# Kernel optimization log

Hardware: AMD Instinct MI355X
Metric: run time of the kernel (lower is better)

## Reference

```python
import jax, jax.numpy as jnp
import numpy as np
import math

# Model dims (from init_kwargs + mamba_ssm Mamba2 defaults)
D_MODEL = 1024
EXPAND = 2
HEADDIM = 64
D_STATE = 64
D_CONV = 4
NGROUPS = 1
D_INNER = EXPAND * D_MODEL            # 2048
NHEADS = D_INNER // HEADDIM           # 32
CONV_DIM = D_INNER + 2 * NGROUPS * D_STATE   # 2176
D_IN_PROJ = 2 * D_INNER + 2 * NGROUPS * D_STATE + NHEADS  # 4256
BATCH, SEQLEN = 4, 2048
RMS_EPS = 1.1920929e-07   # torch.finfo(float32).eps (nn.RMSNorm eps=None)
GNORM_EPS = 1e-5          # mamba_ssm RMSNormGated eps


def _rmsnorm(x, w, eps):
    return x * jax.lax.rsqrt(jnp.mean(x * x, axis=-1, keepdims=True) + eps) * w


def setup_inputs() -> dict:
    key = jax.random.key(0)
    ks = jax.random.split(key, 8)
    x = jax.random.normal(ks[0], (BATCH, SEQLEN, D_MODEL), jnp.float32)
    # router MLP (Linear(d_model,32) -> SiLU -> Linear(32,3))
    r_w1 = jax.random.normal(ks[1], (32, D_MODEL), jnp.float32) / math.sqrt(D_MODEL)
    r_b1 = jnp.zeros((32,), jnp.float32)
    r_w2 = jax.random.normal(ks[2], (3, 32), jnp.float32) / math.sqrt(32)
    r_b2 = jnp.zeros((3,), jnp.float32)
    # Mamba2 params
    in_proj_w = jax.random.normal(ks[3], (D_IN_PROJ, D_MODEL), jnp.float32) / math.sqrt(D_MODEL)
    conv_w = jax.random.normal(ks[4], (CONV_DIM, D_CONV), jnp.float32) * 0.2
    conv_b = jnp.zeros((CONV_DIM,), jnp.float32)
    dt_bias = jax.random.normal(ks[5], (NHEADS,), jnp.float32) * 0.1
    # OrthoSSM multi-scale override: A_log[i] = log(0.001 * 2**i)
    A_log = jnp.log(0.001 * (2.0 ** jnp.arange(NHEADS, dtype=jnp.float32)))
    D_param = jnp.ones((NHEADS,), jnp.float32)
    gnorm_w = jnp.ones((D_INNER,), jnp.float32)
    out_proj_w = jax.random.normal(ks[6], (D_MODEL, D_INNER), jnp.float32) / math.sqrt(D_INNER)
    norm_w = jnp.ones((D_MODEL,), jnp.float32)
    return {"x": x, "norm_w": norm_w, "r_w1": r_w1, "r_b1": r_b1, "r_w2": r_w2,
            "r_b2": r_b2, "in_proj_w": in_proj_w, "conv_w": conv_w, "conv_b": conv_b,
            "dt_bias": dt_bias, "A_log": A_log, "D_param": D_param,
            "gnorm_w": gnorm_w, "out_proj_w": out_proj_w}


def _forward(x, norm_w, r_w1, r_b1, r_w2, r_b2, in_proj_w, conv_w, conv_b,
             dt_bias, A_log, D_param, gnorm_w, out_proj_w):
    B, S, Dm = x.shape
    x_norm = _rmsnorm(x, norm_w, RMS_EPS)
    # --- router: mean-pool -> tiny MLP -> softmax over 3 tiers ---
    h = jax.nn.silu(x_norm.mean(axis=1) @ r_w1.T + r_b1)
    probs = jax.nn.softmax(h @ r_w2.T + r_b2, axis=-1)   # [B,3]
    p_fast = probs[:, 0][:, None, None]
    p_mamba = (probs[:, 1] + probs[:, 2])[:, None, None]
    # --- Mamba2(x_norm) ---
    zxbcdt = x_norm @ in_proj_w.T                         # [B,S,4256]
    z, xBC, dt = jnp.split(zxbcdt, [D_INNER, D_INNER + CONV_DIM], axis=-1)
    # causal depthwise conv1d (kernel 4) + SiLU
    conv = jax.lax.conv_general_dilated(
        xBC.transpose(0, 2, 1), conv_w[:, None, :], (1,), [(D_CONV - 1, 0)],
        feature_group_count=CONV_DIM)                      # [B,CONV_DIM,S]
    xBC = jax.nn.silu(conv.transpose(0, 2, 1) + conv_b)    # [B,S,CONV_DIM]
    xh, Bmat, Cmat = jnp.split(xBC, [D_INNER, D_INNER + NGROUPS * D_STATE], axis=-1)
    xh = xh.reshape(B, S, NHEADS, HEADDIM)                 # [B,S,H,P]
    dt = jax.nn.softplus(dt + dt_bias)                     # [B,S,H]
    A = -jnp.exp(A_log)                                    # [H]
    dA = jnp.exp(dt * A)                                   # [B,S,H]

    def step(hstate, inp):
        dA_t, dt_t, x_t, B_t, C_t = inp
        # hstate: [B,H,P,N]
        hstate = hstate * dA_t[..., None, None] \
                 + (dt_t[..., None] * x_t)[..., None] * B_t[:, None, None, :]
        y_t = jnp.einsum('bhpn,bn->bhp', hstate, C_t)
        return hstate, y_t

    h0 = jnp.zeros((B, NHEADS, HEADDIM, D_STATE), x.dtype)
    xs = (dA.transpose(1, 0, 2), dt.transpose(1, 0, 2), xh.transpose(1, 0, 2, 3),
          Bmat.transpose(1, 0, 2), Cmat.transpose(1, 0, 2))
    _, ys = jax.lax.scan(step, h0, xs)                     # [S,B,H,P]
    y = ys.transpose(1, 0, 2, 3) + D_param[:, None] * xh   # D skip connection
    y = y.reshape(B, S, D_INNER)
    # gated RMSNorm: norm(y * silu(z)) * weight
    yg = y * jax.nn.silu(z)
    yg = _rmsnorm(yg, gnorm_w, GNORM_EPS)
    mamba_out = yg @ out_proj_w.T                          # [B,S,D]
    out = p_fast * x_norm + p_mamba * mamba_out
    return x + out


def reference(x, norm_w, r_w1, r_b1, r_w2, r_b2, in_proj_w, conv_w, conv_b,
              dt_bias, A_log, D_param, gnorm_w, out_proj_w):
    return _forward(x, norm_w, r_w1, r_b1, r_w2, r_b2, in_proj_w, conv_w, conv_b,
                    dt_bias, A_log, D_param, gnorm_w, out_proj_w)
```

## Files before the change

### kernel.cpp

```cpp
#include <hip/hip_runtime.h>
#include <math.h>

typedef __bf16 bf16;
typedef __bf16 bf16x8 __attribute__((ext_vector_type(8)));
typedef __bf16 bf16x4 __attribute__((ext_vector_type(4)));
typedef float f32x4 __attribute__((ext_vector_type(4)));

#define DEV static __device__ __forceinline__
#define AS1 __attribute__((address_space(1)))
#define AS3 __attribute__((address_space(3)))

constexpr int kBatch = 4, kSeq = 2048, kDModel = 1024;
constexpr int kDInner = 2048, kHeads = 32;
constexpr int kConvDim = 2176, kDInProj = 4256, kNPad1 = 4352;
constexpr int kRows = kBatch * kSeq;
constexpr int kChunk = 64, kNChunk = kSeq / kChunk;
constexpr float kRmsEps = 1.1920929e-07f;
constexpr float kGnEps = 1e-5f;
constexpr int kW1Blocks = kNPad1 * kDModel / 256;
constexpr int kW2Blocks = kDModel * kDInner / 1024;

DEV float siluf(float x) { return x / (1.f + expf(-x)); }

DEV float block_reduce_sum(float v, float* red, int tid) {
#pragma unroll
  for (int m = 1; m < 64; m <<= 1) v += __shfl_xor(v, m);
  if ((tid & 63) == 0) red[tid >> 6] = v;
  __syncthreads();
  return red[0] + red[1] + red[2] + red[3];
}

__global__ __launch_bounds__(256) void k_pre(
    const float* __restrict__ x, const float* __restrict__ nw,
    bf16* __restrict__ xnb, float* __restrict__ rs,
    const float* __restrict__ w1, bf16* __restrict__ w1b,
    const float* __restrict__ w2, const float* __restrict__ gw,
    bf16* __restrict__ w2b) {
  const int blk = blockIdx.x;
  const int tid = threadIdx.x;
  if (blk < kRows) {
    const int row = blk;
    float4 v = ((const float4*)(x + (size_t)row * kDModel))[tid];
    __shared__ float red[4];
    float ss = block_reduce_sum(v.x * v.x + v.y * v.y + v.z * v.z + v.w * v.w, red, tid);
    float scale = rsqrtf(ss * (1.f / kDModel) + kRmsEps);
    if (tid == 0) rs[row] = scale;
    float4 wv = ((const float4*)nw)[tid];
    bf16x4 ov;
    ov[0] = (bf16)(v.x * scale * wv.x);
    ov[1] = (bf16)(v.y * scale * wv.y);
    ov[2] = (bf16)(v.z * scale * wv.z);
    ov[3] = (bf16)(v.w * scale * wv.w);
    *(bf16x4*)(xnb + (size_t)row * kDModel + tid * 4) = ov;
  } else if (blk < kRows + kW1Blocks) {
    const size_t idx = (size_t)(blk - kRows) * 256 + tid;
    const int row = (int)(idx >> 10);
    w1b[idx] = (bf16)(row < kDInProj ? w1[idx] : 0.f);
  } else {
    const size_t i4 = (size_t)(blk - kRows - kW1Blocks) * 256 + tid;
    const int k4 = (int)((i4 * 4) & (kDInner - 1));
    float4 v = ((const float4*)w2)[i4];
    float4 g = *(const float4*)(gw + k4);
    bf16x4 o;
    o[0] = (bf16)(v.x * g.x); o[1] = (bf16)(v.y * g.y);
    o[2] = (bf16)(v.z * g.z); o[3] = (bf16)(v.w * g.w);
    ((bf16x4*)w2b)[i4] = o;
  }
}

__global__ __launch_bounds__(128) void k_pool1(const bf16* __restrict__ xnb,
                                               float* __restrict__ part) {
  const int g = blockIdx.x, b = blockIdx.y;
  const int tid = threadIdx.x;
  const bf16* base = xnb + ((size_t)b * kSeq + (size_t)g * 32) * kDModel + tid * 8;
  float acc[8] = {0, 0, 0, 0, 0, 0, 0, 0};
  for (int r = 0; r < 32; ++r) {
    bf16x8 v = *(const bf16x8*)(base + (size_t)r * kDModel);
#pragma unroll
    for (int j = 0; j < 8; ++j) acc[j] += (float)v[j];
  }
  float* o = part + ((size_t)b * 64 + g) * kDModel + tid * 8;
#pragma unroll
  for (int j = 0; j < 8; ++j) o[j] = acc[j];
}

__global__ __launch_bounds__(256) void k_pool2(const float* __restrict__ part,
                                               float* __restrict__ mean) {
  const int idx = blockIdx.x * 256 + threadIdx.x;
  const int b = idx >> 10, d = idx & 1023;
  float s = 0.f;
  for (int g = 0; g < 64; ++g) s += part[((size_t)b * 64 + g) * kDModel + d];
  mean[idx] = s * (1.f / kSeq);
}

__global__ __launch_bounds__(128) void k_router(const float* __restrict__ mean,
                                                const float* __restrict__ w1,
                                                const float* __restrict__ b1,
                                                const float* __restrict__ w2,
                                                const float* __restrict__ b2,
                                                float* __restrict__ pfm) {
  __shared__ float hbuf[4][32];
  __shared__ float logit[4][3];
  const int t = threadIdx.x;
  {
    int b = t >> 5, j = t & 31;
    float s = b1[j];
    for (int d = 0; d < kDModel; ++d) s += mean[b * kDModel + d] * w1[j * kDModel + d];
    hbuf[b][j] = siluf(s);
  }
  __syncthreads();
  if (t < 12) {
    int b = t / 3, k = t % 3;
    float s = b2[k];
    for (int j = 0; j < 32; ++j) s += hbuf[b][j] * w2[k * 32 + j];
    logit[b][k] = s;
  }
  __syncthreads();
  if (t < 4) {
    float m = fmaxf(logit[t][0], fmaxf(logit[t][1], logit[t][2]));
    float e0 = expf(logit[t][0] - m), e1 = expf(logit[t][1] - m), e2 = expf(logit[t][2] - m);
    float inv = 1.f / (e0 + e1 + e2);
    pfm[t] = e0 * inv;
    pfm[4 + t] = (e1 + e2) * inv;
  }
}

template <int WM, int WN, int NF, bool FUSE>
DEV void gemm_body(bf16* lds, float* rs2s,
                   const bf16* __restrict__ A, const bf16* __restrict__ B,
                   bf16* __restrict__ Cb, const float* __restrict__ xres,
                   const float* __restrict__ rs, const float* __restrict__ nw,
                   const float* __restrict__ pfm, float* __restrict__ outf,
                   int K, int Nreal, int ldc, int ntn) {
  constexpr int THREADS = WM * WN * 64;
  constexpr int BM = WM * 64;
  constexpr int BN = WN * NF * 16;
  constexpr int NA = (BM * 4) / THREADS;
  constexpr int NB = (BN * 4) / THREADS;
  constexpr int VMN = NA + NB;
  constexpr int ASZ = (BM / 2) * 64;
  constexpr int BSZ = (BN / 2) * 64;
  const int tid = threadIdx.x;
  const int lane = tid & 63, wid = tid >> 6;
  const int wr = wid / WN, wc = wid % WN;
  const int lr = lane & 15, kb = lane >> 4;
  const int cpx = (int)gridDim.x >> 3;
  const int bid = ((int)blockIdx.x & 7) * cpx + ((int)blockIdx.x >> 3);
  const long n0 = (long)(bid % ntn) * BN;
  const long m0 = (long)(bid / ntn) * BM;

  f32x4 acc[4][NF];
#pragma unroll
  for (int i = 0; i < 4; ++i)
#pragma unroll
    for (int j = 0; j < NF; ++j) acc[i][j] = (f32x4){0.f, 0.f, 0.f, 0.f};
  float ssq[4] = {0.f, 0.f, 0.f, 0.f};

  const int nkt = K >> 5;

#define STAGE(pp, kt)                                                          \
  {                                                                            \
    const long koff = (long)(kt)*32;                                           \
    _Pragma("unroll") for (int j = 0; j < NA; ++j) {                           \
      int idx = j * THREADS + tid;                                             \
      int line = idx >> 3, sp = (idx & 7) ^ (line & 7);                        \
      int row = line * 2 + (sp >> 2), ch = sp & 3;                             \
      __builtin_amdgcn_global_load_lds(                                        \
          (const AS1 void*)(A + (m0 + row) * K + koff + ch * 8),               \
          (AS3 void*)((char*)(lds + (pp)*ASZ) + idx * 16), 16, 0, 0);          \
    }                                                                          \
    _Pragma("unroll") for (int j = 0; j < NB; ++j) {                           \
      int idx = j * THREADS + tid;                                             \
      int line = idx >> 3, sp = (idx & 7) ^ (line & 7);                        \
      int row = line * 2 + (sp >> 2), ch = sp & 3;                             \
      __builtin_amdgcn_global_load_lds(                                        \
          (const AS1 void*)(B + (n0 + row) * K + koff + ch * 8),               \
          (AS3 void*)((char*)(lds + 3 * ASZ + (pp)*BSZ) + idx * 16), 16, 0, 0);\
    }                                                                          \
  }
#define LOFF(r) (((r) >> 1) * 128 + (((((r)&1) << 2) | kb) ^ (((r) >> 1) & 7)) * 16)
#define RDA(pp, r) (*(const bf16x8*)((const char*)(lds + (pp)*ASZ) + LOFF(r)))
#define RDB(pp, r) (*(const bf16x8*)((const char*)(lds + 3 * ASZ + (pp)*BSZ) + LOFF(r)))

  STAGE(0, 0);
  STAGE(1, 1);

  int cur = 0;
  for (int t = 0; t < nkt; ++t) {
    if (t + 2 < nkt) {
      int sb = cur + 2; if (sb >= 3) sb -= 3;
      STAGE(sb, t + 2);
      if constexpr (VMN == 3) asm volatile("s_waitcnt vmcnt(6)" ::: "memory");
      else asm volatile("s_waitcnt vmcnt(8)" ::: "memory");
    } else if (t + 1 < nkt) {
      if constexpr (VMN == 3) asm volatile("s_waitcnt vmcnt(3)" ::: "memory");
      else asm volatile("s_waitcnt vmcnt(4)" ::: "memory");
    } else {
      asm volatile("s_waitcnt vmcnt(0)" ::: "memory");
    }
    __builtin_amdgcn_s_barrier();

    bf16x8 bv[NF], af0, af1, af2, af3;
#pragma unroll
    for (int nf = 0; nf < NF; ++nf) bv[nf] = RDB(cur, wc * (NF * 16) + nf * 16 + lr);
    af0 = RDA(cur, wr * 64 + lr);
    __builtin_amdgcn_sched_barrier(0);
    af1 = RDA(cur, wr * 64 + 16 + lr);
    __builtin_amdgcn_sched_barrier(0);
    asm volatile("s_waitcnt lgkmcnt(1)" ::: "memory");
    __builtin_amdgcn_sched_barrier(0);
    __builtin_amdgcn_s_setprio(1);
#pragma unroll
    for (int nf = 0; nf < NF; ++nf)
      acc[0][nf] = __builtin_amdgcn_mfma_f32_16x16x32_bf16(af0, bv[nf], acc[0][nf], 0, 0, 0);
    af2 = RDA(cur, wr * 64 + 32 + lr);
    af3 = RDA(cur, wr * 64 + 48 + lr);
    __builtin_amdgcn_sched_barrier(0);
    asm volatile("s_waitcnt lgkmcnt(2)" ::: "memory");
    __builtin_amdgcn_sched_barrier(0);
#pragma unroll
    for (int nf = 0; nf < NF; ++nf)
      acc[1][nf] = __builtin_amdgcn_mfma_f32_16x16x32_bf16(af1, bv[nf], acc[1][nf], 0, 0, 0);
    asm volatile("s_waitcnt lgkmcnt(0)" ::: "memory");
    __builtin_amdgcn_sched_barrier(0);
    __builtin_amdgcn_s_barrier();
#pragma unroll
    for (int nf = 0; nf < NF; ++nf)
      acc[2][nf] = __builtin_amdgcn_mfma_f32_16x16x32_bf16(af2, bv[nf], acc[2][nf], 0, 0, 0);
#pragma unroll
    for (int nf = 0; nf < NF; ++nf)
      acc[3][nf] = __builtin_amdgcn_mfma_f32_16x16x32_bf16(af3, bv[nf], acc[3][nf], 0, 0, 0);
    __builtin_amdgcn_s_setprio(0);

    if constexpr (FUSE) {
      if (wc == 0) {
#pragma unroll
        for (int e = 0; e < 8; ++e) {
          float f0 = (float)af0[e], f1 = (float)af1[e];
          float f2 = (float)af2[e], f3 = (float)af3[e];
          ssq[0] = fmaf(f0, f0, ssq[0]);
          ssq[1] = fmaf(f1, f1, ssq[1]);
          ssq[2] = fmaf(f2, f2, ssq[2]);
          ssq[3] = fmaf(f3, f3, ssq[3]);
        }
      }
    }
    cur = cur + 1 == 3 ? 0 : cur + 1;
  }
#undef STAGE
#undef LOFF
#undef RDA
#undef RDB

  const int rr = kb * 4;
  if constexpr (FUSE) {
    if (wc == 0) {
#pragma unroll
      for (int mf = 0; mf < 4; ++mf) {
        float v = ssq[mf];
        v += __shfl_xor(v, 16);
        v += __shfl_xor(v, 32);
        if (kb == 0) rs2s[wr * 64 + mf * 16 + lr] = rsqrtf(v * (1.f / kDInner) + kGnEps);
      }
    }
    __syncthreads();
    const int bx = (int)(m0 >> 11);
    const float pf = pfm[bx], pm = pfm[4 + bx];
#pragma unroll
    for (int mf = 0; mf < 4; ++mf) {
      long rbase = m0 + wr * 64 + mf * 16 + rr;
      float rsv[4], r2v[4];
#pragma unroll
      for (int j = 0; j < 4; ++j) {
        rsv[j] = rs[rbase + j];
        r2v[j] = rs2s[wr * 64 + mf * 16 + rr + j];
      }
#pragma unroll
      for (int nf = 0; nf < NF; ++nf) {
        int col = (int)n0 + wc * (NF * 16) + nf * 16 + lr;
        float wv = nw[col];
#pragma unroll
        for (int j = 0; j < 4; ++j) {
          size_t oi = (size_t)(rbase + j) * kDModel + col;
          float xv = xres[oi];
          outf[oi] = xv + pf * xv * rsv[j] * wv + pm * r2v[j] * acc[mf][nf][j];
        }
      }
    }
  } else {
    __syncthreads();
    bf16* scr = lds + wid * (16 * 72);
    const int srow = lane >> 2, cg = lane & 3;
#pragma unroll
    for (int mf = 0; mf < 4; ++mf) {
#pragma unroll
      for (int nf = 0; nf < NF; ++nf)
#pragma unroll
        for (int j = 0; j < 4; ++j)
          scr[(rr + j) * 72 + nf * 16 + lr] = (bf16)acc[mf][nf][j];
      asm volatile("s_waitcnt lgkmcnt(0)" ::: "memory");
      __builtin_amdgcn_sched_barrier(0);
      int col = (int)n0 + wc * (NF * 16) + cg * 16;
      if (col < Nreal) {
        long grow = m0 + wr * 64 + mf * 16 + srow;
        bf16x8 v0 = *(const bf16x8*)(scr + srow * 72 + cg * 16);
        bf16x8 v1 = *(const bf16x8*)(scr + srow * 72 + cg * 16 + 8);
        *(bf16x8*)(Cb + grow * (long)ldc + col) = v0;
        *(bf16x8*)(Cb + grow * (long)ldc + col + 8) = v1;
      }
      __builtin_amdgcn_sched_barrier(0);
    }
  }
}

__global__ __launch_bounds__(512, 4) void k_gemm_in(
    const bf16* __restrict__ A, const bf16* __restrict__ B,
    bf16* __restrict__ Cb, int K, int Nreal, int ldc, int ntn) {
  constexpr int ASZ = (128 / 2) * 64, BSZ = (256 / 2) * 64;
  __shared__ __align__(16) bf16 lds[3 * ASZ + 3 * BSZ];
  __shared__ float rs2s[128];
  gemm_body<2, 4, 4, false>(lds, rs2s, A, B, Cb, nullptr, nullptr, nullptr,
                            nullptr, nullptr, K, Nreal, ldc, ntn);
}

__global__ __launch_bounds__(256, 4) void k_gemm_out(
    const bf16* __restrict__ A, const bf16* __restrict__ B,
    const float* __restrict__ xres, const float* __restrict__ rs,
    const float* __restrict__ nw, const float* __restrict__ pfm,
    float* __restrict__ outf, int K, int Nreal, int ldc, int ntn) {
  constexpr int ASZ = (64 / 2) * 64, BSZ = (128 / 2) * 64;
  __shared__ __align__(16) bf16 lds[3 * ASZ + 3 * BSZ];
  __shared__ float rs2s[64];
  gemm_body<1, 4, 2, true>(lds, rs2s, A, B, nullptr, xres, rs, nw, pfm, outf,
                           K, Nreal, ldc, ntn);
}

__global__ __launch_bounds__(256) void k_convdt(const bf16* __restrict__ zx,
                                                const float* __restrict__ cw,
                                                const float* __restrict__ cb,
                                                bf16* __restrict__ xbc,
                                                const float* __restrict__ dt_bias,
                                                const float* __restrict__ A_log,
                                                float* __restrict__ dt,
                                                float* __restrict__ ldA) {
  const int gid = blockIdx.x * 256 + threadIdx.x;
  if (gid < kRows * 272) {
    const int row = gid / 272;
    const int cg = gid - row * 272;
    const int c0 = cg * 8;
    const int s = row & (kSeq - 1);
    const bf16* base = zx + (size_t)row * kDInProj + kDInner + c0;
    bf16x8 z8 = {};
    bf16x8 r3 = *(const bf16x8*)(base);
    bf16x8 r2 = (s >= 1) ? *(const bf16x8*)(base - kDInProj) : z8;
    bf16x8 r1 = (s >= 2) ? *(const bf16x8*)(base - 2 * kDInProj) : z8;
    bf16x8 r0 = (s >= 3) ? *(const bf16x8*)(base - 3 * kDInProj) : z8;
    bf16x8 o;
#pragma unroll
    for (int e = 0; e < 8; ++e) {
      float4 w = ((const float4*)cw)[c0 + e];
      float a = cb[c0 + e] + w.x * (float)r0[e] + w.y * (float)r1[e] +
                w.z * (float)r2[e] + w.w * (float)r3[e];
      o[e] = (bf16)siluf(a);
    }
    *(bf16x8*)(xbc + (size_t)row * kConvDim + c0) = o;
  } else {
    const int g2 = gid - kRows * 272;
    const int row = g2 >> 2, grp = g2 & 3;
    bf16x8 r8 = *(const bf16x8*)(zx + (size_t)row * kDInProj + (kDInner + kConvDim) + grp * 8);
#pragma unroll
    for (int e = 0; e < 8; ++e) {
      int hh = grp * 8 + e;
      float raw = (float)r8[e] + dt_bias[hh];
      float dtv = (raw > 20.f) ? raw : log1pf(expf(raw));
      dt[row * kHeads + hh] = dtv;
      ldA[row * kHeads + hh] = dtv * -expf(A_log[hh]);
    }
  }
}

__global__ __launch_bounds__(256) void k_chunkA(
    const bf16* __restrict__ xbc, const float* __restrict__ dtb,
    const float* __restrict__ ldab, float* __restrict__ cumbuf,
    float* __restrict__ Tc, bf16* __restrict__ Sbuf) {
  const int c = blockIdx.x, h = blockIdx.y, b = blockIdx.z;
  const int tid = threadIdx.x;
  const int w = tid >> 6, lane = tid & 63, lr = lane & 15, kb = lane >> 4;
  const int rr = kb * 4;
  const int t0 = c * kChunk;
  __shared__ bf16 Bl[64 * 72], XT[64 * 72], WBT[64 * 72];
  __shared__ float w_s[64];

  {
    int s = tid >> 2, q = tid & 3;
    const bf16* rowp = xbc + ((size_t)b * kSeq + t0 + s) * kConvDim;
    bf16x8 x0 = *(const bf16x8*)(rowp + h * 64 + q * 16);
    bf16x8 x1 = *(const bf16x8*)(rowp + h * 64 + q * 16 + 8);
    bf16x8 b0 = *(const bf16x8*)(rowp + kDInner + q * 16);
    bf16x8 b1 = *(const bf16x8*)(rowp + kDInner + q * 16 + 8);
    *(bf16x8*)(Bl + s * 72 + q * 16) = b0;
    *(bf16x8*)(Bl + s * 72 + q * 16 + 8) = b1;
#pragma unroll
    for (int e = 0; e < 8; ++e) XT[(q * 16 + e) * 72 + s] = x0[e];
#pragma unroll
    for (int e = 0; e < 8; ++e) XT[(q * 16 + 8 + e) * 72 + s] = x1[e];
  }
  if (tid < 64) {
    size_t di = ((size_t)b * kSeq + t0 + tid) * kHeads + h;
    float v = ldab[di];
    float dtv = dtb[di];
#pragma unroll
    for (int o = 1; o < 64; o <<= 1) {
      float u = __shfl_up(v, o);
      if (lane >= o) v += u;
    }
    float tot = __shfl(v, 63);
    w_s[tid] = expf(tot - v) * dtv;
    cumbuf[(((size_t)b * kHeads + h) * kNChunk + c) * 64 + tid] = v;
    if (tid == 63) Tc[(b * kHeads + h) * kNChunk + c] = expf(v);
  }
  __syncthreads();

#pragma unroll
  for (int i = 0; i < 16; ++i) {
    int e = i * 256 + tid;
    int n = e >> 6, s = e & 63;
    WBT[n * 72 + s] = (bf16)((float)Bl[s * 72 + n] * w_s[s]);
  }
  __syncthreads();

  f32x4 s4[4];
#pragma unroll
  for (int nt = 0; nt < 4; ++nt) s4[nt] = (f32x4){0.f, 0.f, 0.f, 0.f};
#pragma unroll
  for (int kk = 0; kk < 2; ++kk) {
    bf16x8 a = *(const bf16x8*)(XT + (w * 16 + lr) * 72 + kk * 32 + kb * 8);
#pragma unroll
    for (int nt = 0; nt < 4; ++nt) {
      bf16x8 bb = *(const bf16x8*)(WBT + (nt * 16 + lr) * 72 + kk * 32 + kb * 8);
      s4[nt] = __builtin_amdgcn_mfma_f32_16x16x32_bf16(a, bb, s4[nt], 0, 0, 0);
    }
  }
#pragma unroll
  for (int nt = 0; nt < 4; ++nt)
#pragma unroll
    for (int j = 0; j < 4; ++j)
      Bl[(w * 16 + rr + j) * 72 + nt * 16 + lr] = (bf16)s4[nt][j];
  __syncthreads();
  {
    int row = tid >> 2, cg = tid & 3;
    const size_t sbase = (((size_t)b * kHeads + h) * kNChunk + c) * 4096;
    bf16x8 u0 = *(const bf16x8*)(Bl + row * 72 + cg * 16);
    bf16x8 u1 = *(const bf16x8*)(Bl + row * 72 + cg * 16 + 8);
    bf16* sdst = Sbuf + sbase + row * 64 + cg * 16;
    *(bf16x8*)sdst = u0;
    *(bf16x8*)(sdst + 8) = u1;
  }
}

__global__ __launch_bounds__(256) void k_chunkB(bf16* __restrict__ S,
                                                const float* __restrict__ Tc) {
  const int gid = blockIdx.x * 256 + threadIdx.x;
  const int bh = gid >> 10;
  const int pn = (gid & 1023) << 2;
  bf16* base = S + (size_t)bh * kNChunk * 4096 + pn;
  const float* tc = Tc + bh * kNChunk;
  float4 hh = {0.f, 0.f, 0.f, 0.f};
  bf16x4 s = *(const bf16x4*)(base);
  for (int c = 0; c < kNChunk; ++c) {
    bf16x4 sn = {};
    if (c + 1 < kNChunk) sn = *(const bf16x4*)(base + (size_t)(c + 1) * 4096);
    float t = tc[c];
    bf16x4 ho;
    ho[0] = (bf16)hh.x; ho[1] = (bf16)hh.y; ho[2] = (bf16)hh.z; ho[3] = (bf16)hh.w;
    *(bf16x4*)(base + (size_t)c * 4096) = ho;
    hh.x = t * hh.x + (float)s[0];
    hh.y = t * hh.y + (float)s[1];
    hh.z = t * hh.z + (float)s[2];
    hh.w = t * hh.w + (float)s[3];
    s = sn;
  }
}

__global__ __launch_bounds__(256) void k_chunkC(
    const bf16* __restrict__ xbc, const bf16* __restrict__ zx,
    const float* __restrict__ dtb, const float* __restrict__ cumbuf,
    const bf16* __restrict__ hs, const float* __restrict__ Dp,
    bf16* __restrict__ yb) {
  const int c = blockIdx.x, h = blockIdx.y, b = blockIdx.z;
  const int tid = threadIdx.x;
  const int w = tid >> 6, lane = tid & 63, lr = lane & 15, kb = lane >> 4;
  const int rr = kb * 4;
  const int t0 = c * kChunk;
  __shared__ bf16 Bl[64 * 72], Cl[64 * 72], XT[64 * 72], Ml[64 * 72];
  __shared__ float cum_s[64], dt_s[64], ecum[64];
  __shared__ float scrf[64 * 68];

  {
    int s = tid >> 2, q = tid & 3;
    const bf16* rowp = xbc + ((size_t)b * kSeq + t0 + s) * kConvDim;
    bf16x8 x0 = *(const bf16x8*)(rowp + h * 64 + q * 16);
    bf16x8 x1 = *(const bf16x8*)(rowp + h * 64 + q * 16 + 8);
    bf16x8 b0 = *(const bf16x8*)(rowp + kDInner + q * 16);
    bf16x8 b1 = *(const bf16x8*)(rowp + kDInner + q * 16 + 8);
    bf16x8 c0 = *(const bf16x8*)(rowp + kDInner + 64 + q * 16);
    bf16x8 c1 = *(const bf16x8*)(rowp + kDInner + 64 + q * 16 + 8);
    *(bf16x8*)(Bl + s * 72 + q * 16) = b0;
    *(bf16x8*)(Bl + s * 72 + q * 16 + 8) = b1;
    *(bf16x8*)(Cl + s * 72 + q * 16) = c0;
    *(bf16x8*)(Cl + s * 72 + q * 16 + 8) = c1;
#pragma unroll
    for (int e = 0; e < 8; ++e) XT[(q * 16 + e) * 72 + s] = x0[e];
#pragma unroll
    for (int e = 0; e < 8; ++e) XT[(q * 16 + 8 + e) * 72 + s] = x1[e];
  }
  if (tid < 64) {
    size_t di = ((size_t)b * kSeq + t0 + tid) * kHeads + h;
    float cv = cumbuf[(((size_t)b * kHeads + h) * kNChunk + c) * 64 + tid];
    cum_s[tid] = cv;
    ecum[tid] = expf(cv);
    dt_s[tid] = dtb[di];
  }
  __syncthreads();

  f32x4 g[4];
#pragma unroll
  for (int nt = 0; nt < 4; ++nt) g[nt] = (f32x4){0.f, 0.f, 0.f, 0.f};
#pragma unroll
  for (int kk = 0; kk < 2; ++kk) {
    bf16x8 a = *(const bf16x8*)(Cl + (w * 16 + lr) * 72 + kk * 32 + kb * 8);
#pragma unroll
    for (int nt = 0; nt < 4; ++nt) {
      bf16x8 bb = *(const bf16x8*)(Bl + (nt * 16 + lr) * 72 + kk * 32 + kb * 8);
      g[nt] = __builtin_amdgcn_mfma_f32_16x16x32_bf16(a, bb, g[nt], 0, 0, 0);
    }
  }
#pragma unroll
  for (int nt = 0; nt < 4; ++nt)
#pragma unroll
    for (int j = 0; j < 4; ++j) {
      int tt = w * 16 + rr + j, ss = nt * 16 + lr;
      float m = (ss <= tt) ? g[nt][j] * expf(cum_s[tt] - cum_s[ss]) * dt_s[ss] : 0.f;
      Ml[tt * 72 + ss] = (bf16)m;
    }
  __syncthreads();

  f32x4 y4[4];
#pragma unroll
  for (int pt = 0; pt < 4; ++pt) y4[pt] = (f32x4){0.f, 0.f, 0.f, 0.f};
#pragma unroll
  for (int kk = 0; kk < 2; ++kk) {
    bf16x8 a = *(const bf16x8*)(Ml + (w * 16 + lr) * 72 + kk * 32 + kb * 8);
#pragma unroll
    for (int pt = 0; pt < 4; ++pt) {
      bf16x8 bb = *(const bf16x8*)(XT + (pt * 16 + lr) * 72 + kk * 32 + kb * 8);
      y4[pt] = __builtin_amdgcn_mfma_f32_16x16x32_bf16(a, bb, y4[pt], 0, 0, 0);
    }
  }
  const bf16* hbase = hs + (((size_t)b * kHeads + h) * kNChunk + c) * 4096;
  f32x4 acc2[4];
#pragma unroll
  for (int pt = 0; pt < 4; ++pt) acc2[pt] = (f32x4){0.f, 0.f, 0.f, 0.f};
#pragma unroll
  for (int kk = 0; kk < 2; ++kk) {
    bf16x8 a = *(const bf16x8*)(Cl + (w * 16 + lr) * 72 + kk * 32 + kb * 8);
#pragma unroll
    for (int pt = 0; pt < 4; ++pt) {
      bf16x8 bb = *(const bf16x8*)(hbase + (pt * 16 + lr) * 64 + kk * 32 + kb * 8);
      acc2[pt] = __builtin_amdgcn_mfma_f32_16x16x32_bf16(a, bb, acc2[pt], 0, 0, 0);
    }
  }
#pragma unroll
  for (int pt = 0; pt < 4; ++pt)
#pragma unroll
    for (int j = 0; j < 4; ++j) {
      int tt = w * 16 + rr + j;
      scrf[tt * 68 + pt * 16 + lr] = y4[pt][j] + ecum[tt] * acc2[pt][j];
    }
  __syncthreads();
  {
    const float Dh = Dp[h];
    int row = tid >> 2, cg = tid & 3;
    size_t ri = (size_t)b * kSeq + t0 + row;
    const float* sp = scrf + row * 68 + cg * 16;
    bf16* yp = yb + ri * kDInner + h * 64 + cg * 16;
    const bf16* xp = xbc + ri * kConvDim + h * 64 + cg * 16;
    const bf16* zp = zx + ri * kDInProj + h * 64 + cg * 16;
#pragma unroll
    for (int half = 0; half < 2; ++half) {
      bf16x8 xv = *(const bf16x8*)(xp + half * 8);
      bf16x8 zv = *(const bf16x8*)(zp + half * 8);
      bf16x8 o;
#pragma unroll
      for (int e = 0; e < 8; ++e) {
        float yfull = sp[half * 8 + e] + Dh * (float)xv[e];
        o[e] = (bf16)(yfull * siluf((float)zv[e]));
      }
      *(bf16x8*)(yp + half * 8) = o;
    }
  }
}

extern "C" void kernel_launch(void* const* d_in, const int* in_sizes, int n_in,
                              void* d_out, int out_size, void* d_ws, size_t ws_size,
                              hipStream_t stream) {
  const float* x = (const float*)d_in[0];
  const float* norm_w = (const float*)d_in[1];
  const float* r_w1 = (const float*)d_in[2];
  const float* r_b1 = (const float*)d_in[3];
  const float* r_w2 = (const float*)d_in[4];
  const float* r_b2 = (const float*)d_in[5];
  const float* in_proj_w = (const float*)d_in[6];
  const float* conv_w = (const float*)d_in[7];
  const float* conv_b = (const float*)d_in[8];
  const float* dt_bias = (const float*)d_in[9];
  const float* A_log = (const float*)d_in[10];
  const float* D_param = (const float*)d_in[11];
  const float* gnorm_w = (const float*)d_in[12];
  const float* out_proj_w = (const float*)d_in[13];
  float* out = (float*)d_out;
  char* ws = (char*)d_ws;

  bf16* xnb     = (bf16*)(ws + 0);
  bf16* w1b     = (bf16*)(ws + 16777216);
  bf16* zx      = (bf16*)(ws + 25690112);
  bf16* xbc     = (bf16*)(ws + 95420416);
  float* dtb    = (float*)(ws + 131072000);
  float* ldab   = (float*)(ws + 132120576);
  float* cumbuf = (float*)(ws + 133169152);
  float* Tcb    = (float*)(ws + 134217728);
  bf16* yb      = (bf16*)(ws + 134234112);
  bf16* Sbuf    = (bf16*)(ws + 167788544);
  bf16* w2b     = (bf16*)(ws + 201342976);
  float* part   = (float*)(ws + 205537280);
  float* meanb  = (float*)(ws + 206585856);
  float* pfm    = (float*)(ws + 206602240);
  float* rsb    = (float*)(ws + 206602368);

  k_pre<<<kRows + kW1Blocks + kW2Blocks, 256, 0, stream>>>(
      x, norm_w, xnb, rsb, in_proj_w, w1b, out_proj_w, gnorm_w, w2b);
  k_pool1<<<dim3(64, 4), 128, 0, stream>>>(xnb, part);
  k_pool2<<<16, 256, 0, stream>>>(part, meanb);
  k_router<<<1, 128, 0, stream>>>(meanb, r_w1, r_b1, r_w2, r_b2, pfm);
  k_gemm_in<<<(kRows / 128) * (kNPad1 / 256), 512, 0, stream>>>(
      xnb, w1b, zx, kDModel, kDInProj, kDInProj, kNPad1 / 256);
  k_convdt<<<(kRows * 272 + kRows * 4) / 256, 256, 0, stream>>>(
      zx, conv_w, conv_b, xbc, dt_bias, A_log, dtb, ldab);
  k_chunkA<<<dim3(kNChunk, kHeads, kBatch), 256, 0, stream>>>(
      xbc, dtb, ldab, cumbuf, Tcb, Sbuf);
  k_chunkB<<<512, 256, 0, stream>>>(Sbuf, Tcb);
  k_chunkC<<<dim3(kNChunk, kHeads, kBatch), 256, 0, stream>>>(
      xbc, zx, dtb, cumbuf, Sbuf, D_param, yb);
  k_gemm_out<<<(kRows / 64) * (kDModel / 128), 256, 0, stream>>>(
      yb, w2b, x, rsb, norm_w, pfm, out,
      kDInner, kDModel, kDModel, kDModel / 128);
}
```

Baseline: 343.5 us.

## Fold router pooling into existing kernels and enlarge out-projection GEMM tile

Removes three small router kernels. The sequence-mean pooling becomes extra blocks appended to the in-projection GEMM grid. The pool reduction becomes extra threads in the conv/dt kernel, and the router MLP and softmax become an extra block of the chunk-state scan kernel. This cuts launch overhead and serial tiny kernels. Separately, the out-projection GEMM tile grows from 64x128 to 128x128 with a 2x2 wave layout, which improves operand reuse but halves the block count.

```diff
diff --git a/kernel.cpp b/kernel.cpp
--- a/kernel.cpp
+++ b/kernel.cpp
@@ -19,6 +19,8 @@
 constexpr float kGnEps = 1e-5f;
 constexpr int kW1Blocks = kNPad1 * kDModel / 256;
 constexpr int kW2Blocks = kDModel * kDInner / 1024;
+constexpr int kGemm1Blocks = (kRows / 128) * (kNPad1 / 256);
+constexpr int kPool1Blocks = 256;
 
 DEV float siluf(float x) { return x / (1.f + expf(-x)); }
 
@@ -68,70 +70,13 @@
   }
 }
 
-__global__ __launch_bounds__(128) void k_pool1(const bf16* __restrict__ xnb,
-                                               float* __restrict__ part) {
-  const int g = blockIdx.x, b = blockIdx.y;
-  const int tid = threadIdx.x;
-  const bf16* base = xnb + ((size_t)b * kSeq + (size_t)g * 32) * kDModel + tid * 8;
-  float acc[8] = {0, 0, 0, 0, 0, 0, 0, 0};
-  for (int r = 0; r < 32; ++r) {
-    bf16x8 v = *(const bf16x8*)(base + (size_t)r * kDModel);
-#pragma unroll
-    for (int j = 0; j < 8; ++j) acc[j] += (float)v[j];
-  }
-  float* o = part + ((size_t)b * 64 + g) * kDModel + tid * 8;
-#pragma unroll
-  for (int j = 0; j < 8; ++j) o[j] = acc[j];
-}
-
-__global__ __launch_bounds__(256) void k_pool2(const float* __restrict__ part,
-                                               float* __restrict__ mean) {
-  const int idx = blockIdx.x * 256 + threadIdx.x;
-  const int b = idx >> 10, d = idx & 1023;
-  float s = 0.f;
-  for (int g = 0; g < 64; ++g) s += part[((size_t)b * 64 + g) * kDModel + d];
-  mean[idx] = s * (1.f / kSeq);
-}
-
-__global__ __launch_bounds__(128) void k_router(const float* __restrict__ mean,
-                                                const float* __restrict__ w1,
-                                                const float* __restrict__ b1,
-                                                const float* __restrict__ w2,
-                                                const float* __restrict__ b2,
-                                                float* __restrict__ pfm) {
-  __shared__ float hbuf[4][32];
-  __shared__ float logit[4][3];
-  const int t = threadIdx.x;
-  {
-    int b = t >> 5, j = t & 31;
-    float s = b1[j];
-    for (int d = 0; d < kDModel; ++d) s += mean[b * kDModel + d] * w1[j * kDModel + d];
-    hbuf[b][j] = siluf(s);
-  }
-  __syncthreads();
-  if (t < 12) {
-    int b = t / 3, k = t % 3;
-    float s = b2[k];
-    for (int j = 0; j < 32; ++j) s += hbuf[b][j] * w2[k * 32 + j];
-    logit[b][k] = s;
-  }
-  __syncthreads();
-  if (t < 4) {
-    float m = fmaxf(logit[t][0], fmaxf(logit[t][1], logit[t][2]));
-    float e0 = expf(logit[t][0] - m), e1 = expf(logit[t][1] - m), e2 = expf(logit[t][2] - m);
-    float inv = 1.f / (e0 + e1 + e2);
-    pfm[t] = e0 * inv;
-    pfm[4 + t] = (e1 + e2) * inv;
-  }
-}
-
 template <int WM, int WN, int NF, bool FUSE>
 DEV void gemm_body(bf16* lds, float* rs2s,
                    const bf16* __restrict__ A, const bf16* __restrict__ B,
                    bf16* __restrict__ Cb, const float* __restrict__ xres,
                    const float* __restrict__ rs, const float* __restrict__ nw,
                    const float* __restrict__ pfm, float* __restrict__ outf,
-                   int K, int Nreal, int ldc, int ntn) {
+                   int K, int Nreal, int ldc, int ntn, int nblk) {
   constexpr int THREADS = WM * WN * 64;
   constexpr int BM = WM * 64;
   constexpr int BN = WN * NF * 16;
@@ -144,7 +89,7 @@
   const int lane = tid & 63, wid = tid >> 6;
   const int wr = wid / WN, wc = wid % WN;
   const int lr = lane & 15, kb = lane >> 4;
-  const int cpx = (int)gridDim.x >> 3;
+  const int cpx = nblk >> 3;
   const int bid = ((int)blockIdx.x & 7) * cpx + ((int)blockIdx.x >> 3);
   const long n0 = (long)(bid % ntn) * BN;
   const long m0 = (long)(bid / ntn) * BM;
@@ -315,12 +260,30 @@
 
 __global__ __launch_bounds__(512, 4) void k_gemm_in(
     const bf16* __restrict__ A, const bf16* __restrict__ B,
-    bf16* __restrict__ Cb, int K, int Nreal, int ldc, int ntn) {
+    bf16* __restrict__ Cb, float* __restrict__ part4,
+    int K, int Nreal, int ldc, int ntn, int ngemm) {
   constexpr int ASZ = (128 / 2) * 64, BSZ = (256 / 2) * 64;
   __shared__ __align__(16) bf16 lds[3 * ASZ + 3 * BSZ];
   __shared__ float rs2s[128];
+  if ((int)blockIdx.x >= ngemm) {
+    const int blk2 = (int)blockIdx.x - ngemm;
+    const int b = blk2 >> 6, g = blk2 & 63;
+    const int tid = threadIdx.x;
+    const int cs = (tid & 127) * 8, rseg = tid >> 7;
+    const bf16* base = A + ((size_t)b * kSeq + g * 32 + rseg * 8) * kDModel + cs;
+    float acc[8] = {0, 0, 0, 0, 0, 0, 0, 0};
+    for (int r = 0; r < 8; ++r) {
+      bf16x8 v = *(const bf16x8*)(base + (size_t)r * kDModel);
+#pragma unroll
+      for (int j = 0; j < 8; ++j) acc[j] += (float)v[j];
+    }
+    float* o = part4 + ((size_t)((b * 64 + g) * 4 + rseg)) * kDModel + cs;
+#pragma unroll
+    for (int j = 0; j < 8; ++j) o[j] = acc[j];
+    return;
+  }
   gemm_body<2, 4, 4, false>(lds, rs2s, A, B, Cb, nullptr, nullptr, nullptr,
-                            nullptr, nullptr, K, Nreal, ldc, ntn);
+                            nullptr, nullptr, K, Nreal, ldc, ntn, ngemm);
 }
 
 __global__ __launch_bounds__(256, 4) void k_gemm_out(
@@ -328,11 +291,11 @@
     const float* __restrict__ xres, const float* __restrict__ rs,
     const float* __restrict__ nw, const float* __restrict__ pfm,
     float* __restrict__ outf, int K, int Nreal, int ldc, int ntn) {
-  constexpr int ASZ = (64 / 2) * 64, BSZ = (128 / 2) * 64;
+  constexpr int ASZ = (128 / 2) * 64, BSZ = (128 / 2) * 64;
   __shared__ __align__(16) bf16 lds[3 * ASZ + 3 * BSZ];
-  __shared__ float rs2s[64];
-  gemm_body<1, 4, 2, true>(lds, rs2s, A, B, nullptr, xres, rs, nw, pfm, outf,
-                           K, Nreal, ldc, ntn);
+  __shared__ float rs2s[128];
+  gemm_body<2, 2, 4, true>(lds, rs2s, A, B, nullptr, xres, rs, nw, pfm, outf,
+                           K, Nreal, ldc, ntn, (int)gridDim.x);
 }
 
 __global__ __launch_bounds__(256) void k_convdt(const bf16* __restrict__ zx,
@@ -342,7 +305,9 @@
                                                 const float* __restrict__ dt_bias,
                                                 const float* __restrict__ A_log,
                                                 float* __restrict__ dt,
-                                                float* __restrict__ ldA) {
+                                                float* __restrict__ ldA,
+                                                const float* __restrict__ part4,
+                                                float* __restrict__ meanb) {
   const int gid = blockIdx.x * 256 + threadIdx.x;
   if (gid < kRows * 272) {
     const int row = gid / 272;
@@ -364,7 +329,7 @@
       o[e] = (bf16)siluf(a);
     }
     *(bf16x8*)(xbc + (size_t)row * kConvDim + c0) = o;
-  } else {
+  } else if (gid < kRows * 272 + kRows * 4) {
     const int g2 = gid - kRows * 272;
     const int row = g2 >> 2, grp = g2 & 3;
     bf16x8 r8 = *(const bf16x8*)(zx + (size_t)row * kDInProj + (kDInner + kConvDim) + grp * 8);
@@ -376,6 +341,13 @@
       dt[row * kHeads + hh] = dtv;
       ldA[row * kHeads + hh] = dtv * -expf(A_log[hh]);
     }
+  } else {
+    const int i2 = gid - (kRows * 272 + kRows * 4);
+    const int b = i2 >> 10, d = i2 & 1023;
+    const float* p = part4 + (size_t)b * 256 * kDModel + d;
+    float s = 0.f;
+    for (int j = 0; j < 256; ++j) s += p[(size_t)j * kDModel];
+    meanb[i2] = s * (1.f / kSeq);
   }
 }
 
@@ -458,8 +430,38 @@
   }
 }
 
-__global__ __launch_bounds__(256) void k_chunkB(bf16* __restrict__ S,
-                                                const float* __restrict__ Tc) {
+__global__ __launch_bounds__(256) void k_chunkB(
+    bf16* __restrict__ S, const float* __restrict__ Tc,
+    const float* __restrict__ mean, const float* __restrict__ w1,
+    const float* __restrict__ b1, const float* __restrict__ w2,
+    const float* __restrict__ b2, float* __restrict__ pfm) {
+  __shared__ float hbuf[4][32];
+  __shared__ float logit[4][3];
+  if (blockIdx.x == 512) {
+    const int t = threadIdx.x;
+    if (t < 128) {
+      int b = t >> 5, j = t & 31;
+      float s = b1[j];
+      for (int d = 0; d < kDModel; ++d) s += mean[b * kDModel + d] * w1[j * kDModel + d];
+      hbuf[b][j] = siluf(s);
+    }
+    __syncthreads();
+    if (t < 12) {
+      int b = t / 3, k = t % 3;
+      float s = b2[k];
+      for (int j = 0; j < 32; ++j) s += hbuf[b][j] * w2[k * 32 + j];
+      logit[b][k] = s;
+    }
+    __syncthreads();
+    if (t < 4) {
+      float m = fmaxf(logit[t][0], fmaxf(logit[t][1], logit[t][2]));
+      float e0 = expf(logit[t][0] - m), e1 = expf(logit[t][1] - m), e2 = expf(logit[t][2] - m);
+      float inv = 1.f / (e0 + e1 + e2);
+      pfm[t] = e0 * inv;
+      pfm[4 + t] = (e1 + e2) * inv;
+    }
+    return;
+  }
   const int gid = blockIdx.x * 256 + threadIdx.x;
   const int bh = gid >> 10;
   const int pn = (gid & 1023) << 2;
@@ -632,26 +634,23 @@
   bf16* yb      = (bf16*)(ws + 134234112);
   bf16* Sbuf    = (bf16*)(ws + 167788544);
   bf16* w2b     = (bf16*)(ws + 201342976);
-  float* part   = (float*)(ws + 205537280);
-  float* meanb  = (float*)(ws + 206585856);
-  float* pfm    = (float*)(ws + 206602240);
-  float* rsb    = (float*)(ws + 206602368);
+  float* part4  = (float*)(ws + 205537280);
+  float* meanb  = (float*)(ws + 209731584);
+  float* pfm    = (float*)(ws + 209747968);
+  float* rsb    = (float*)(ws + 209748096);
 
   k_pre<<<kRows + kW1Blocks + kW2Blocks, 256, 0, stream>>>(
       x, norm_w, xnb, rsb, in_proj_w, w1b, out_proj_w, gnorm_w, w2b);
-  k_pool1<<<dim3(64, 4), 128, 0, stream>>>(xnb, part);
-  k_pool2<<<16, 256, 0, stream>>>(part, meanb);
-  k_router<<<1, 128, 0, stream>>>(meanb, r_w1, r_b1, r_w2, r_b2, pfm);
-  k_gemm_in<<<(kRows / 128) * (kNPad1 / 256), 512, 0, stream>>>(
-      xnb, w1b, zx, kDModel, kDInProj, kDInProj, kNPad1 / 256);
-  k_convdt<<<(kRows * 272 + kRows * 4) / 256, 256, 0, stream>>>(
-      zx, conv_w, conv_b, xbc, dt_bias, A_log, dtb, ldab);
+  k_gemm_in<<<kGemm1Blocks + kPool1Blocks, 512, 0, stream>>>(
+      xnb, w1b, zx, part4, kDModel, kDInProj, kDInProj, kNPad1 / 256, kGemm1Blocks);
+  k_convdt<<<(kRows * 272 + kRows * 4 + 4096) / 256, 256, 0, stream>>>(
+      zx, conv_w, conv_b, xbc, dt_bias, A_log, dtb, ldab, part4, meanb);
   k_chunkA<<<dim3(kNChunk, kHeads, kBatch), 256, 0, stream>>>(
       xbc, dtb, ldab, cumbuf, Tcb, Sbuf);
-  k_chunkB<<<512, 256, 0, stream>>>(Sbuf, Tcb);
+  k_chunkB<<<513, 256, 0, stream>>>(Sbuf, Tcb, meanb, r_w1, r_b1, r_w2, r_b2, pfm);
   k_chunkC<<<dim3(kNChunk, kHeads, kBatch), 256, 0, stream>>>(
       xbc, zx, dtb, cumbuf, Sbuf, D_param, yb);
-  k_gemm_out<<<(kRows / 64) * (kDModel / 128), 256, 0, stream>>>(
+  k_gemm_out<<<(kRows / 128) * (kDModel / 128), 256, 0, stream>>>(
       yb, w2b, x, rsb, norm_w, pfm, out,
       kDInner, kDModel, kDModel, kDModel / 128);
 }
```

Result: no change. 345.4 us (+0.6%).

## Rewrite in-proj GEMM with 32x32x16 MFMA and retile out-proj GEMM

Applied to the files above, without the earlier changes.

Replaces the templated in-projection GEMM with a dedicated kernel that uses 32x32x16 bf16 MFMA tiles, 64x64 per-wave output tiles and a remapped block order for better L2 locality. It also retiles the out-projection GEMM from 64x128 to 128x128 blocks with a 2x2 wave layout, halving its grid. The shared GEMM body now issues all LDS reads before the MFMAs instead of interleaving them. Larger MFMA tiles cut LDS traffic per flop, but the out-proj grid becomes smaller and the loss of read/compute interleaving may expose LDS latency.

```diff
diff --git a/kernel.cpp b/kernel.cpp
--- a/kernel.cpp
+++ b/kernel.cpp
@@ -5,6 +5,7 @@
 typedef __bf16 bf16x8 __attribute__((ext_vector_type(8)));
 typedef __bf16 bf16x4 __attribute__((ext_vector_type(4)));
 typedef float f32x4 __attribute__((ext_vector_type(4)));
+typedef float f32x16 __attribute__((ext_vector_type(16)));
 
 #define DEV static __device__ __forceinline__
 #define AS1 __attribute__((address_space(1)))
@@ -125,6 +126,126 @@
   }
 }
 
+__global__ __launch_bounds__(512, 4) void k_gemm_in(
+    const bf16* __restrict__ A, const bf16* __restrict__ B,
+    bf16* __restrict__ Cb, int K, int Nreal, int ldc, int ntn) {
+  constexpr int ASZ = 64 * 64;
+  constexpr int BSZ = 128 * 64;
+  __shared__ __align__(16) bf16 lds[3 * ASZ + 3 * BSZ];
+  const int tid = threadIdx.x;
+  const int lane = tid & 63, wid = tid >> 6;
+  const int wr = wid >> 2, wc = wid & 3;
+  const int l31 = lane & 31, l5 = lane >> 5;
+  const int cpx = (int)gridDim.x >> 3;
+  const int bid = ((int)blockIdx.x & 7) * cpx + ((int)blockIdx.x >> 3);
+  const long n0 = (long)(bid % ntn) * 256;
+  const long m0 = (long)(bid / ntn) * 128;
+
+  f32x16 acc00 = {}, acc01 = {}, acc10 = {}, acc11 = {};
+
+  const int nkt = K >> 5;
+
+#define STAGE(pp, kt)                                                          \
+  {                                                                            \
+    const long koff = (long)(kt)*32;                                           \
+    {                                                    \
+      int idx = tid;                                                           \
+      int line = idx >> 3, sp = (idx & 7) ^ (line & 7);                        \
+      int row = line * 2 + (sp >> 2), ch = sp & 3;                             \
+      __builtin_amdgcn_global_load_lds(                                        \
+          (const AS1 void*)(A + (m0 + row) * K + koff + ch * 8),               \
+          (AS3 void*)((char*)(lds + (pp)*ASZ) + idx * 16), 16, 0, 0);          \
+    }                                                                          \
+    _Pragma("unroll") for (int j = 0; j < 2; ++j) {            \
+      int idx = j * 512 + tid;                                                 \
+      int line = idx >> 3, sp = (idx & 7) ^ (line & 7);                        \
+      int row = line * 2 + (sp >> 2), ch = sp & 3;                             \
+      __builtin_amdgcn_global_load_lds(                                        \
+          (const AS1 void*)(B + (n0 + row) * K + koff + ch * 8),               \
+          (AS3 void*)((char*)(lds + 3 * ASZ + (pp)*BSZ) + idx * 16), 16, 0, 0);\
+    }                                                                          \
+  }
+#define LOFF(r, c) (((r) >> 1) * 128 + (((((r)&1) << 2) | (c)) ^ (((r) >> 1) & 7)) * 16)
+#define RDA(pp, r, c) (*(const bf16x8*)((const char*)(lds + (pp)*ASZ) + LOFF(r, c)))
+#define RDB(pp, r, c) (*(const bf16x8*)((const char*)(lds + 3 * ASZ + (pp)*BSZ) + LOFF(r, c)))
+
+  STAGE(0, 0);
+  STAGE(1, 1);
+
+  int cur = 0;
+  for (int t = 0; t < nkt; ++t) {
+    if (t + 2 < nkt) {
+      int sb = cur + 2; if (sb >= 3) sb -= 3;
+      STAGE(sb, t + 2);
+      asm volatile("s_waitcnt vmcnt(6)" ::: "memory");
+    } else if (t + 1 < nkt) {
+      asm volatile("s_waitcnt vmcnt(3)" ::: "memory");
+    } else {
+      asm volatile("s_waitcnt vmcnt(0)" ::: "memory");
+    }
+    __builtin_amdgcn_s_barrier();
+
+    bf16x8 a00 = RDA(cur, wr * 64 + l31, l5);
+    bf16x8 a01 = RDA(cur, wr * 64 + l31, 2 + l5);
+    bf16x8 a10 = RDA(cur, wr * 64 + 32 + l31, l5);
+    bf16x8 a11 = RDA(cur, wr * 64 + 32 + l31, 2 + l5);
+    bf16x8 b00 = RDB(cur, wc * 64 + l31, l5);
+    bf16x8 b01 = RDB(cur, wc * 64 + l31, 2 + l5);
+    bf16x8 b10 = RDB(cur, wc * 64 + 32 + l31, l5);
+    bf16x8 b11 = RDB(cur, wc * 64 + 32 + l31, 2 + l5);
+    asm volatile("s_waitcnt lgkmcnt(0)" ::: "memory");
+    __builtin_amdgcn_sched_barrier(0);
+    __builtin_amdgcn_s_barrier();
+
+    __builtin_amdgcn_s_setprio(1);
+    acc00 = __builtin_amdgcn_mfma_f32_32x32x16_bf16(a00, b00, acc00, 0, 0, 0);
+    acc01 = __builtin_amdgcn_mfma_f32_32x32x16_bf16(a00, b10, acc01, 0, 0, 0);
+    acc10 = __builtin_amdgcn_mfma_f32_32x32x16_bf16(a10, b00, acc10, 0, 0, 0);
+    acc11 = __builtin_amdgcn_mfma_f32_32x32x16_bf16(a10, b10, acc11, 0, 0, 0);
+    acc00 = __builtin_amdgcn_mfma_f32_32x32x16_bf16(a01, b01, acc00, 0, 0, 0);
+    acc01 = __builtin_amdgcn_mfma_f32_32x32x16_bf16(a01, b11, acc01, 0, 0, 0);
+    acc10 = __builtin_amdgcn_mfma_f32_32x32x16_bf16(a11, b01, acc10, 0, 0, 0);
+    acc11 = __builtin_amdgcn_mfma_f32_32x32x16_bf16(a11, b11, acc11, 0, 0, 0);
+    __builtin_amdgcn_s_setprio(0);
+    cur = cur + 1 == 3 ? 0 : cur + 1;
+  }
+#undef STAGE
+#undef LOFF
+#undef RDA
+#undef RDB
+
+  __syncthreads();
+  bf16* scr = lds + wid * (32 * 72);
+  const int srow = lane >> 1, scoff = (lane & 1) * 32;
+#pragma unroll
+  for (int mf = 0; mf < 2; ++mf) {
+#pragma unroll
+    for (int reg = 0; reg < 16; ++reg) {
+      int rl = (reg & 3) + 8 * (reg >> 2) + 4 * l5;
+      float v0 = mf == 0 ? acc00[reg] : acc10[reg];
+      float v1 = mf == 0 ? acc01[reg] : acc11[reg];
+      scr[rl * 72 + l31] = (bf16)v0;
+      scr[rl * 72 + 32 + l31] = (bf16)v1;
+    }
+    asm volatile("s_waitcnt lgkmcnt(0)" ::: "memory");
+    __builtin_amdgcn_sched_barrier(0);
+    int col = (int)n0 + wc * 64 + scoff;
+    if (col < Nreal) {
+      long grow = m0 + wr * 64 + mf * 32 + srow;
+      bf16x8 u0 = *(const bf16x8*)(scr + srow * 72 + scoff);
+      bf16x8 u1 = *(const bf16x8*)(scr + srow * 72 + scoff + 8);
+      bf16x8 u2 = *(const bf16x8*)(scr + srow * 72 + scoff + 16);
+      bf16x8 u3 = *(const bf16x8*)(scr + srow * 72 + scoff + 24);
+      bf16* dst = Cb + grow * (long)ldc + col;
+      *(bf16x8*)dst = u0;
+      *(bf16x8*)(dst + 8) = u1;
+      *(bf16x8*)(dst + 16) = u2;
+      *(bf16x8*)(dst + 24) = u3;
+    }
+    __builtin_amdgcn_sched_barrier(0);
+  }
+}
+
 template <int WM, int WN, int NF, bool FUSE>
 DEV void gemm_body(bf16* lds, float* rs2s,
                    const bf16* __restrict__ A, const bf16* __restrict__ B,
@@ -204,33 +325,12 @@
 #pragma unroll
     for (int nf = 0; nf < NF; ++nf) bv[nf] = RDB(cur, wc * (NF * 16) + nf * 16 + lr);
     af0 = RDA(cur, wr * 64 + lr);
-    __builtin_amdgcn_sched_barrier(0);
     af1 = RDA(cur, wr * 64 + 16 + lr);
-    __builtin_amdgcn_sched_barrier(0);
-    asm volatile("s_waitcnt lgkmcnt(1)" ::: "memory");
-    __builtin_amdgcn_sched_barrier(0);
-    __builtin_amdgcn_s_setprio(1);
-#pragma unroll
-    for (int nf = 0; nf < NF; ++nf)
-      acc[0][nf] = __builtin_amdgcn_mfma_f32_16x16x32_bf16(af0, bv[nf], acc[0][nf], 0, 0, 0);
     af2 = RDA(cur, wr * 64 + 32 + lr);
     af3 = RDA(cur, wr * 64 + 48 + lr);
-    __builtin_amdgcn_sched_barrier(0);
-    asm volatile("s_waitcnt lgkmcnt(2)" ::: "memory");
-    __builtin_amdgcn_sched_barrier(0);
-#pragma unroll
-    for (int nf = 0; nf < NF; ++nf)
-      acc[1][nf] = __builtin_amdgcn_mfma_f32_16x16x32_bf16(af1, bv[nf], acc[1][nf], 0, 0, 0);
     asm volatile("s_waitcnt lgkmcnt(0)" ::: "memory");
     __builtin_amdgcn_sched_barrier(0);
     __builtin_amdgcn_s_barrier();
-#pragma unroll
-    for (int nf = 0; nf < NF; ++nf)
-      acc[2][nf] = __builtin_amdgcn_mfma_f32_16x16x32_bf16(af2, bv[nf], acc[2][nf], 0, 0, 0);
-#pragma unroll
-    for (int nf = 0; nf < NF; ++nf)
-      acc[3][nf] = __builtin_amdgcn_mfma_f32_16x16x32_bf16(af3, bv[nf], acc[3][nf], 0, 0, 0);
-    __builtin_amdgcn_s_setprio(0);
 
     if constexpr (FUSE) {
       if (wc == 0) {
@@ -245,6 +345,20 @@
         }
       }
     }
+    __builtin_amdgcn_s_setprio(1);
+#pragma unroll
+    for (int nf = 0; nf < NF; ++nf)
+      acc[0][nf] = __builtin_amdgcn_mfma_f32_16x16x32_bf16(af0, bv[nf], acc[0][nf], 0, 0, 0);
+#pragma unroll
+    for (int nf = 0; nf < NF; ++nf)
+      acc[1][nf] = __builtin_amdgcn_mfma_f32_16x16x32_bf16(af1, bv[nf], acc[1][nf], 0, 0, 0);
+#pragma unroll
+    for (int nf = 0; nf < NF; ++nf)
+      acc[2][nf] = __builtin_amdgcn_mfma_f32_16x16x32_bf16(af2, bv[nf], acc[2][nf], 0, 0, 0);
+#pragma unroll
+    for (int nf = 0; nf < NF; ++nf)
+      acc[3][nf] = __builtin_amdgcn_mfma_f32_16x16x32_bf16(af3, bv[nf], acc[3][nf], 0, 0, 0);
+    __builtin_amdgcn_s_setprio(0);
     cur = cur + 1 == 3 ? 0 : cur + 1;
   }
 #undef STAGE
@@ -313,25 +427,15 @@
   }
 }
 
-__global__ __launch_bounds__(512, 4) void k_gemm_in(
-    const bf16* __restrict__ A, const bf16* __restrict__ B,
-    bf16* __restrict__ Cb, int K, int Nreal, int ldc, int ntn) {
-  constexpr int ASZ = (128 / 2) * 64, BSZ = (256 / 2) * 64;
-  __shared__ __align__(16) bf16 lds[3 * ASZ + 3 * BSZ];
-  __shared__ float rs2s[128];
-  gemm_body<2, 4, 4, false>(lds, rs2s, A, B, Cb, nullptr, nullptr, nullptr,
-                            nullptr, nullptr, K, Nreal, ldc, ntn);
-}
-
 __global__ __launch_bounds__(256, 4) void k_gemm_out(
     const bf16* __restrict__ A, const bf16* __restrict__ B,
     const float* __restrict__ xres, const float* __restrict__ rs,
     const float* __restrict__ nw, const float* __restrict__ pfm,
     float* __restrict__ outf, int K, int Nreal, int ldc, int ntn) {
-  constexpr int ASZ = (64 / 2) * 64, BSZ = (128 / 2) * 64;
+  constexpr int ASZ = (128 / 2) * 64, BSZ = (128 / 2) * 64;
   __shared__ __align__(16) bf16 lds[3 * ASZ + 3 * BSZ];
-  __shared__ float rs2s[64];
-  gemm_body<1, 4, 2, true>(lds, rs2s, A, B, nullptr, xres, rs, nw, pfm, outf,
+  __shared__ float rs2s[128];
+  gemm_body<2, 2, 4, true>(lds, rs2s, A, B, nullptr, xres, rs, nw, pfm, outf,
                            K, Nreal, ldc, ntn);
 }
 
@@ -651,7 +755,7 @@
   k_chunkB<<<512, 256, 0, stream>>>(Sbuf, Tcb);
   k_chunkC<<<dim3(kNChunk, kHeads, kBatch), 256, 0, stream>>>(
       xbc, zx, dtb, cumbuf, Sbuf, D_param, yb);
-  k_gemm_out<<<(kRows / 64) * (kDModel / 128), 256, 0, stream>>>(
+  k_gemm_out<<<(kRows / 128) * (kDModel / 128), 256, 0, stream>>>(
       yb, w2b, x, rsb, norm_w, pfm, out,
       kDInner, kDModel, kDModel, kDModel / 128);
 }
```

Result: slower. 367.1 us (+6.9%).
